# Kernel optimization log

Hardware: AMD Instinct MI355X
Metric: run time of the kernel (lower is better)

Reference implementation:

```python
import jax, jax.numpy as jnp
import numpy as np

N = 10000
E = 160000
NUM_GRAPHS = 64
HEADS = 4
HID = 256
PROJ = HEADS * HID  # 1024


def setup_inputs() -> dict:
    key = jax.random.key(0)
    ks = jax.random.split(key, 16)
    s = 0.02
    return {
        "x": jax.random.normal(ks[0], (N, 1024), jnp.float32),
        "edge_index": jax.random.randint(ks[1], (2, E), 0, N, jnp.int64) if jax.config.jax_enable_x64 else jax.random.randint(ks[1], (2, E), 0, N).astype(jnp.int32),
        "batch": jnp.sort(jax.random.randint(ks[2], (N,), 0, NUM_GRAPHS)),
        "proj_W": jax.random.normal(ks[3], (1024, PROJ), jnp.float32) * s,
        "proj_b": jnp.zeros((PROJ,), jnp.float32),
        "gat_W": jax.random.normal(ks[4], (3, PROJ, PROJ), jnp.float32) * s,
        "gat_att_src": jax.random.normal(ks[5], (3, HEADS, HID), jnp.float32) * s,
        "gat_att_dst": jax.random.normal(ks[6], (3, HEADS, HID), jnp.float32) * s,
        "gat_bias": jnp.zeros((3, PROJ), jnp.float32),
        "norm_gamma": jnp.ones((3, PROJ), jnp.float32),
        "norm_beta": jnp.zeros((3, PROJ), jnp.float32),
        "pool_W1": jax.random.normal(ks[7], (PROJ, PROJ // 2), jnp.float32) * s,
        "pool_b1": jnp.zeros((PROJ // 2,), jnp.float32),
        "pool_W2": jax.random.normal(ks[8], (PROJ // 2, 1), jnp.float32) * s,
        "pool_b2": jnp.zeros((1,), jnp.float32),
        "cls_W1": jax.random.normal(ks[9], (PROJ, PROJ // 2), jnp.float32) * s,
        "cls_b1": jnp.zeros((PROJ // 2,), jnp.float32),
        "cls_W2": jax.random.normal(ks[10], (PROJ // 2, 14), jnp.float32) * s,
        "cls_b2": jnp.zeros((14,), jnp.float32),
    }


def _segment_softmax(e, seg, num_segments):
    # numerically stable softmax over segments; e: (E, ...) scores
    m = jax.ops.segment_max(e, seg, num_segments=num_segments)
    e = jnp.exp(e - m[seg])
    s = jax.ops.segment_sum(e, seg, num_segments=num_segments)
    return e / (s[seg] + 1e-16)


def _layer_norm(x, gamma, beta):
    mu = jnp.mean(x, axis=-1, keepdims=True)
    var = jnp.var(x, axis=-1, keepdims=True)
    return (x - mu) * jax.lax.rsqrt(var + 1e-5) * gamma + beta


def _gat_conv(x, src, dst, W, a_src, a_dst, b):
    n = x.shape[0]
    h = (x @ W).reshape(n, HEADS, HID)          # (N,H,D)
    alpha_s = jnp.einsum('nhd,hd->nh', h, a_src)  # (N,H)
    alpha_d = jnp.einsum('nhd,hd->nh', h, a_dst)
    e = jax.nn.leaky_relu(alpha_s[src] + alpha_d[dst], 0.2)  # (E,H)
    alpha = _segment_softmax(e, dst, n)
    msg = h[src] * alpha[:, :, None]             # (E,H,D)
    out = jax.ops.segment_sum(msg, dst, num_segments=n)
    return out.reshape(n, PROJ) + b


def _forward(x, edge_index, batch, proj_W, proj_b, gat_W, gat_att_src, gat_att_dst,
             gat_bias, norm_gamma, norm_beta, pool_W1, pool_b1, pool_W2, pool_b2,
             cls_W1, cls_b1, cls_W2, cls_b2):
    n = x.shape[0]
    # GATConv default add_self_loops=True
    loops = jnp.arange(n, dtype=edge_index.dtype)
    src = jnp.concatenate([edge_index[0], loops])
    dst = jnp.concatenate([edge_index[1], loops])

    x = x @ proj_W + proj_b
    for i in range(3):
        h = jax.nn.elu(_gat_conv(x, src, dst, gat_W[i], gat_att_src[i], gat_att_dst[i], gat_bias[i]))
        x = _layer_norm(x + h, norm_gamma[i], norm_beta[i])  # dropout is identity in eval

    # attention pooling
    scores = (jnp.tanh(x @ pool_W1 + pool_b1) @ pool_W2 + pool_b2).squeeze(-1)  # (N,)
    w = _segment_softmax(scores, batch, NUM_GRAPHS)
    pooled = jax.ops.segment_sum(x * w[:, None], batch, num_segments=NUM_GRAPHS)  # (G,PROJ)

    hid = jax.nn.gelu(pooled @ cls_W1 + cls_b1, approximate=False)
    return hid @ cls_W2 + cls_b2  # (G,14)


def reference(x, edge_index, batch, proj_W, proj_b, gat_W, gat_att_src, gat_att_dst,
              gat_bias, norm_gamma, norm_beta, pool_W1, pool_b1, pool_W2, pool_b2,
              cls_W1, cls_b1, cls_W2, cls_b2):
    return _forward(x, edge_index, batch, proj_W, proj_b, gat_W, gat_att_src,
                    gat_att_dst, gat_bias, norm_gamma, norm_beta, pool_W1, pool_b1,
                    pool_W2, pool_b2, cls_W1, cls_b1, cls_W2, cls_b2)
```

## Files before the change

kernel.cpp:

```cpp
#include <hip/hip_runtime.h>
#include <hip/hip_bf16.h>
#include <hip/hip_fp16.h>
#include <math.h>

#define NPROJ 1024
#define NHEADS 4
#define NHID 256
#define NGRAPH 64

typedef _Float16 half8 __attribute__((ext_vector_type(8)));
typedef _Float16 half4v __attribute__((ext_vector_type(4)));
typedef float floatx4 __attribute__((ext_vector_type(4)));

#define GLD_LDS16(g, l)                                                        \
  __builtin_amdgcn_global_load_lds(                                            \
      (const __attribute__((address_space(1))) unsigned int*)(g),              \
      (__attribute__((address_space(3))) unsigned int*)(l), 16, 0, 0)

template<int ACT, int OUT>
__global__ __launch_bounds__(256, 4) void gemm_mfma(
    const _Float16* __restrict__ A, const _Float16* __restrict__ BT,
    const float* __restrict__ bias, float* __restrict__ Cf,
    _Float16* __restrict__ Ch, _Float16* __restrict__ Cl,
    int M, int Nc, int lgn, int mpad8)
{
  __shared__ __align__(16) _Float16 ldsA[128 * 64];
  __shared__ __align__(16) _Float16 ldsB[128 * 64];

  const int id  = blockIdx.x;
  const int xcd = id & 7;
  const int kk  = id >> 3;
  const int bx  = kk & ((1 << lgn) - 1);
  const int by  = xcd * mpad8 + (kk >> lgn);
  const int m0  = by * 128, n0 = bx * 128;
  if (m0 >= M) return;

  const int tid  = threadIdx.x;
  const int lane = tid & 63;
  const int wave = tid >> 6;
  const int wm = wave >> 1, wn = wave & 1;

  const int srow = tid >> 3;
  const int kc8  = (((tid & 7) ^ ((tid >> 3) & 7)) << 3);
  const int wb16 = (tid & ~63) * 16;

  floatx4 acc[4][4] = {};

  const int l15 = lane & 15;
  const int swz = (l15 & 7) << 4;
  const int kbyte0 = (lane >> 4) * 16;

  auto STAGE = [&](int t) {
    const int k0 = t << 6;
#pragma unroll
    for (int r = 0; r < 4; ++r) {
      int rowA = m0 + r * 32 + srow;
      rowA = rowA < M ? rowA : (M - 1);
      GLD_LDS16(A + (size_t)rowA * 1024 + k0 + kc8,
                (char*)ldsA + r * 4096 + wb16);
      GLD_LDS16(BT + (size_t)(n0 + r * 32 + srow) * 1024 + k0 + kc8,
                (char*)ldsB + r * 4096 + wb16);
    }
  };

  STAGE(0);
  __syncthreads();

  for (int t = 0; t < 16; ++t) {
    const int koff0 = kbyte0 ^ swz;
    half8 a0[4], b0[4];
#pragma unroll
    for (int i = 0; i < 4; ++i)
      a0[i] = *(const half8*)((const char*)ldsA +
                              (wm * 64 + i * 16 + l15) * 128 + koff0);
#pragma unroll
    for (int j = 0; j < 4; ++j)
      b0[j] = *(const half8*)((const char*)ldsB +
                              (wn * 64 + j * 16 + l15) * 128 + koff0);
#pragma unroll
    for (int i = 0; i < 4; ++i)
#pragma unroll
      for (int j = 0; j < 4; ++j)
        acc[i][j] = __builtin_amdgcn_mfma_f32_16x16x32_f16(a0[i], b0[j],
                                                           acc[i][j], 0, 0, 0);

    const int koff1 = (64 + kbyte0) ^ swz;
    half8 a1[4], b1[4];
#pragma unroll
    for (int i = 0; i < 4; ++i)
      a1[i] = *(const half8*)((const char*)ldsA +
                              (wm * 64 + i * 16 + l15) * 128 + koff1);
#pragma unroll
    for (int j = 0; j < 4; ++j)
      b1[j] = *(const half8*)((const char*)ldsB +
                              (wn * 64 + j * 16 + l15) * 128 + koff1);
    __syncthreads();
    if (t < 15) STAGE(t + 1);

#pragma unroll
    for (int i = 0; i < 4; ++i)
#pragma unroll
      for (int j = 0; j < 4; ++j)
        acc[i][j] = __builtin_amdgcn_mfma_f32_16x16x32_f16(a1[i], b1[j],
                                                           acc[i][j], 0, 0, 0);

    if (t < 15) __syncthreads();
  }

  const int rbase = (lane >> 4) * 4;
#pragma unroll
  for (int j = 0; j < 4; ++j) {
    const int col = n0 + wn * 64 + j * 16 + l15;
    const float bv = bias ? bias[col] : 0.f;
#pragma unroll
    for (int i = 0; i < 4; ++i) {
      const int gm0 = m0 + wm * 64 + i * 16 + rbase;
#pragma unroll
      for (int r = 0; r < 4; ++r) {
        const int gm = gm0 + r;
        if (gm >= M) continue;
        float v = acc[i][j][r] + bv;
        if (ACT == 1) v = tanhf(v);
        if (OUT == 1) {
          _Float16 hh = (_Float16)v;
          Ch[(size_t)gm * Nc + col] = hh;
          Cl[(size_t)gm * Nc + col] = (_Float16)(v - (float)hh);
        } else if (OUT == 2) {
          Ch[(size_t)gm * Nc + col] = (_Float16)v;
        } else {
          Cf[(size_t)gm * Nc + col] = v;
        }
      }
    }
  }
}

__global__ void k_tof16(const float* __restrict__ in, _Float16* __restrict__ h,
                        int L8) {
  int i = blockIdx.x * 256 + threadIdx.x;
  if (i >= L8) return;
  const float4* p = (const float4*)(in + (size_t)i * 8);
  float4 v0 = p[0], v1 = p[1];
  float vv[8] = {v0.x, v0.y, v0.z, v0.w, v1.x, v1.y, v1.z, v1.w};
  half8 hv;
#pragma unroll
  for (int j = 0; j < 8; ++j) hv[j] = (_Float16)vv[j];
  *(half8*)(h + (size_t)i * 8) = hv;
}

__global__ __launch_bounds__(256) void k_transT(const float* __restrict__ in,
                                                _Float16* __restrict__ hT,
                                                int K, int Nc) {
  __shared__ float t[32][33];
  const int tx = threadIdx.x & 31, ty = threadIdx.x >> 5;
  const int c0 = blockIdx.x * 32, k0 = blockIdx.y * 32;
#pragma unroll
  for (int r = 0; r < 4; ++r)
    t[ty + 8 * r][tx] = in[(size_t)(k0 + ty + 8 * r) * Nc + c0 + tx];
  __syncthreads();
#pragma unroll
  for (int r = 0; r < 4; ++r) {
    float v = t[tx][ty + 8 * r];
    int oc = c0 + ty + 8 * r;
    hT[(size_t)oc * K + k0 + tx] = (_Float16)v;
  }
}

__global__ void k_init_counts(int* cnt, int n) {
  int i = blockIdx.x * 256 + threadIdx.x;
  if (i < n) cnt[i] = 1;
}

__global__ void k_count(const int* __restrict__ dst, int* cnt, int e) {
  int i = blockIdx.x * 256 + threadIdx.x;
  if (i < e) atomicAdd(&cnt[dst[i]], 1);
}

__global__ __launch_bounds__(1024) void k_scan(const int* __restrict__ cnt,
                                               int* __restrict__ rowstart,
                                               int* __restrict__ cursor, int n) {
  __shared__ int buf[1024];
  __shared__ int carry;
  int t = threadIdx.x;
  if (t == 0) carry = 0;
  __syncthreads();
  for (int base = 0; base < n; base += 1024) {
    int x = (base + t < n) ? cnt[base + t] : 0;
    buf[t] = x;
    __syncthreads();
    for (int off = 1; off < 1024; off <<= 1) {
      int v = (t >= off) ? buf[t - off] : 0;
      __syncthreads();
      buf[t] += v;
      __syncthreads();
    }
    int c0 = carry;
    int excl = buf[t] - x + c0;
    if (base + t < n) { rowstart[base + t] = excl; cursor[base + t] = excl; }
    __syncthreads();
    if (t == 0) carry = c0 + buf[1023];
    __syncthreads();
  }
  if (t == 0) rowstart[n] = carry;
}

__global__ void k_fill(const int* __restrict__ src, const int* __restrict__ dst,
                       int* cursor, int* __restrict__ col, int e) {
  int i = blockIdx.x * 256 + threadIdx.x;
  if (i < e) {
    int p = atomicAdd(&cursor[dst[i]], 1);
    col[p] = src[i];
  }
}

__global__ void k_fill_self(int* cursor, int* __restrict__ col, int n) {
  int i = blockIdx.x * 256 + threadIdx.x;
  if (i < n) {
    int p = atomicAdd(&cursor[i], 1);
    col[p] = i;
  }
}

__global__ __launch_bounds__(256) void k_alpha(
    const _Float16* __restrict__ h, const float* __restrict__ a_src,
    const float* __restrict__ a_dst, float* __restrict__ as_out,
    float* __restrict__ ad_out) {
  int n = blockIdx.x, t = threadIdx.x;
  const int wv = t >> 6, ln = t & 63;
  const int cb = wv * 256 + 4 * ln;
  half4v v = *(const half4v*)(h + (size_t)n * NPROJ + cb);
  float4 s4 = *(const float4*)(a_src + cb);
  float4 d4 = *(const float4*)(a_dst + cb);
  float vv[4] = {(float)v[0], (float)v[1], (float)v[2], (float)v[3]};
  float ss = vv[0] * s4.x + vv[1] * s4.y + vv[2] * s4.z + vv[3] * s4.w;
  float sd = vv[0] * d4.x + vv[1] * d4.y + vv[2] * d4.z + vv[3] * d4.w;
#pragma unroll
  for (int off = 32; off > 0; off >>= 1) {
    ss += __shfl_down(ss, off);
    sd += __shfl_down(sd, off);
  }
  if (ln == 0) {
    as_out[n * 4 + wv] = ss;
    ad_out[n * 4 + wv] = sd;
  }
}

__device__ __forceinline__ float lrelu02(float x) {
  return x > 0.f ? x : 0.2f * x;
}

__global__ __launch_bounds__(256) void k_aggregate_ln(
    const _Float16* __restrict__ h, const float* __restrict__ as_,
    const float* __restrict__ ad_, const int* __restrict__ rowstart,
    const int* __restrict__ col, const float* __restrict__ bias,
    const float* __restrict__ gamma, const float* __restrict__ beta,
    _Float16* __restrict__ xh, _Float16* __restrict__ xl) {
  __shared__ float sred[8];

  const int n = blockIdx.x, t = threadIdx.x;
  const int wv = t >> 6, l = t & 63;
  const int rs = rowstart[n], re = rowstart[n + 1];
  const float adn = ad_[n * 4 + wv];

  float mx = -1e30f;
  for (int e = rs + l; e < re; e += 64)
    mx = fmaxf(mx, lrelu02(as_[(size_t)col[e] * 4 + wv] + adn));
#pragma unroll
  for (int off = 32; off > 0; off >>= 1)
    mx = fmaxf(mx, __shfl_xor(mx, off));

  float sm = 0.f;
  for (int e = rs + l; e < re; e += 64)
    sm += expf(lrelu02(as_[(size_t)col[e] * 4 + wv] + adn) - mx);
#pragma unroll
  for (int off = 32; off > 0; off >>= 1)
    sm += __shfl_xor(sm, off);
  const float Sinv = 1.f / (sm + 1e-16f);

  const int cb = wv * 256 + 4 * l;
  float acc[4] = {0.f, 0.f, 0.f, 0.f};
  for (int c0 = rs; c0 < re; c0 += 64) {
    const int idx = c0 + l;
    float w_l = 0.f;
    int s_l = 0;
    if (idx < re) {
      s_l = col[idx];
      w_l = expf(lrelu02(as_[(size_t)s_l * 4 + wv] + adn) - mx) * Sinv;
    }
    const int cnt = min(64, re - c0);
    int e = 0;
    for (; e + 3 < cnt; e += 4) {
      float w0 = __shfl(w_l, e + 0), w1 = __shfl(w_l, e + 1);
      float w2 = __shfl(w_l, e + 2), w3 = __shfl(w_l, e + 3);
      int s0 = __shfl(s_l, e + 0), s1 = __shfl(s_l, e + 1);
      int s2 = __shfl(s_l, e + 2), s3 = __shfl(s_l, e + 3);
      half4v h0 = *(const half4v*)(h + (size_t)s0 * NPROJ + cb);
      half4v h1 = *(const half4v*)(h + (size_t)s1 * NPROJ + cb);
      half4v h2 = *(const half4v*)(h + (size_t)s2 * NPROJ + cb);
      half4v h3 = *(const half4v*)(h + (size_t)s3 * NPROJ + cb);
#pragma unroll
      for (int j = 0; j < 4; ++j) {
        acc[j] = fmaf(w0, (float)h0[j], acc[j]);
        acc[j] = fmaf(w1, (float)h1[j], acc[j]);
        acc[j] = fmaf(w2, (float)h2[j], acc[j]);
        acc[j] = fmaf(w3, (float)h3[j], acc[j]);
      }
    }
    for (; e < cnt; ++e) {
      const float w = __shfl(w_l, e);
      const int s = __shfl(s_l, e);
      half4v hv = *(const half4v*)(h + (size_t)s * NPROJ + cb);
      acc[0] = fmaf(w, (float)hv[0], acc[0]);
      acc[1] = fmaf(w, (float)hv[1], acc[1]);
      acc[2] = fmaf(w, (float)hv[2], acc[2]);
      acc[3] = fmaf(w, (float)hv[3], acc[3]);
    }
  }

  const size_t base = (size_t)n * NPROJ + cb;
  float4 b4 = *(const float4*)(bias + cb);
  float bb[4] = {b4.x, b4.y, b4.z, b4.w};
  half4v xhv = *(const half4v*)(xh + base);
  half4v xlv = *(const half4v*)(xl + base);
  float v[4];
  float sum = 0.f, sumsq = 0.f;
#pragma unroll
  for (int j = 0; j < 4; ++j) {
    float u = acc[j] + bb[j];
    u = u > 0.f ? u : expm1f(u);
    u += (float)xhv[j] + (float)xlv[j];
    v[j] = u;
    sum += u;
    sumsq += u * u;
  }
#pragma unroll
  for (int off = 32; off > 0; off >>= 1) {
    sum += __shfl_xor(sum, off);
    sumsq += __shfl_xor(sumsq, off);
  }
  if (l == 0) {
    sred[wv] = sum;
    sred[4 + wv] = sumsq;
  }
  __syncthreads();
  const float tsum = sred[0] + sred[1] + sred[2] + sred[3];
  const float tssq = sred[4] + sred[5] + sred[6] + sred[7];
  const float mu = tsum * (1.f / 1024.f);
  const float var = tssq * (1.f / 1024.f) - mu * mu;
  const float rstd = rsqrtf(var + 1e-5f);

  float4 g4 = *(const float4*)(gamma + cb);
  float4 e4 = *(const float4*)(beta + cb);
  float gg[4] = {g4.x, g4.y, g4.z, g4.w};
  float ee[4] = {e4.x, e4.y, e4.z, e4.w};
  half4v oh, ol;
#pragma unroll
  for (int j = 0; j < 4; ++j) {
    float y = (v[j] - mu) * rstd * gg[j] + ee[j];
    _Float16 hh = (_Float16)y;
    oh[j] = hh;
    ol[j] = (_Float16)(y - (float)hh);
  }
  *(half4v*)(xh + base) = oh;
  *(half4v*)(xl + base) = ol;
}

__global__ void k_scores(const float* __restrict__ tb,
                         const float* __restrict__ W2,
                         const float* __restrict__ b2,
                         float* __restrict__ scores, int N) {
  int n = blockIdx.x, lane = threadIdx.x;
  float s = 0.f;
  for (int k = lane; k < 512; k += 64) s = fmaf(tb[(size_t)n * 512 + k], W2[k], s);
  for (int off = 32; off > 0; off >>= 1) s += __shfl_down(s, off);
  if (lane == 0) scores[n] = s + b2[0];
}

__global__ void k_grange_init(int* gstart, int* gend, int N) {
  int g = threadIdx.x;
  if (g < NGRAPH) { gstart[g] = N; gend[g] = 0; }
}

__global__ void k_grange_mark(const int* __restrict__ batch, int* gstart,
                              int* gend, int N) {
  int n = blockIdx.x * 256 + threadIdx.x;
  if (n >= N) return;
  int b = batch[n];
  if (n == 0 || batch[n - 1] != b) gstart[b] = n;
  if (n == N - 1 || batch[n + 1] != b) gend[b] = n + 1;
}

__global__ __launch_bounds__(256) void k_pool(
    const float* __restrict__ scores, const _Float16* __restrict__ xh,
    const _Float16* __restrict__ xl, const int* __restrict__ gstart,
    const int* __restrict__ gend, float* __restrict__ pooled) {
  __shared__ float red[256];
  __shared__ float wt[256];
  __shared__ float m_s, s_s;
  int g = blockIdx.x, t = threadIdx.x;
  int rs = gstart[g], re = gend[g];

  float mx = -1e30f;
  for (int i = rs + t; i < re; i += 256) mx = fmaxf(mx, scores[i]);
  red[t] = mx;
  __syncthreads();
  for (int s = 128; s > 0; s >>= 1) {
    if (t < s) red[t] = fmaxf(red[t], red[t + s]);
    __syncthreads();
  }
  if (t == 0) m_s = red[0];
  __syncthreads();
  float m = m_s;

  float sm = 0.f;
  for (int i = rs + t; i < re; i += 256) sm += expf(scores[i] - m);
  red[t] = sm;
  __syncthreads();
  for (int s = 128; s > 0; s >>= 1) {
    if (t < s) red[t] += red[t + s];
    __syncthreads();
  }
  if (t == 0) s_s = red[0] + 1e-16f;
  __syncthreads();
  float sden = s_s;

  float acc[4] = {0.f, 0.f, 0.f, 0.f};
  for (int c0 = rs; c0 < re; c0 += 256) {
    int cnt = min(256, re - c0);
    if (t < cnt) wt[t] = expf(scores[c0 + t] - m) / sden;
    __syncthreads();
    for (int e = 0; e < cnt; ++e) {
      float w = wt[e];
      size_t base = (size_t)(c0 + e) * NPROJ + 4 * t;
      half4v hv = *(const half4v*)(xh + base);
      half4v lv = *(const half4v*)(xl + base);
#pragma unroll
      for (int j = 0; j < 4; ++j)
        acc[j] = fmaf(w, (float)hv[j] + (float)lv[j], acc[j]);
    }
    __syncthreads();
  }
#pragma unroll
  for (int j = 0; j < 4; ++j) pooled[(size_t)g * NPROJ + 4 * t + j] = acc[j];
}

__global__ __launch_bounds__(256) void k_cls1(const float* __restrict__ pooled,
                                              const float* __restrict__ W1,
                                              const float* __restrict__ b1,
                                              float* __restrict__ hid) {
  __shared__ float p[1024];
  int g = blockIdx.y;
  int colc = blockIdx.x * 256 + threadIdx.x;
  for (int k = threadIdx.x; k < 1024; k += 256) p[k] = pooled[(size_t)g * 1024 + k];
  __syncthreads();
  float s = 0.f;
  for (int k = 0; k < 1024; ++k) s = fmaf(p[k], W1[(size_t)k * 512 + colc], s);
  s += b1[colc];
  s = 0.5f * s * (1.f + erff(s * 0.70710678118654752f));
  hid[(size_t)g * 512 + colc] = s;
}

__global__ void k_cls2(const float* __restrict__ hid,
                       const float* __restrict__ W2,
                       const float* __restrict__ b2, float* __restrict__ out) {
  int o = blockIdx.x, g = blockIdx.y, lane = threadIdx.x;
  float s = 0.f;
  for (int k = lane; k < 512; k += 64) s = fmaf(hid[(size_t)g * 512 + k], W2[k * 14 + o], s);
  for (int off = 32; off > 0; off >>= 1) s += __shfl_down(s, off);
  if (lane == 0) out[g * 14 + o] = s + b2[o];
}

extern "C" void kernel_launch(void* const* d_in, const int* in_sizes, int n_in,
                              void* d_out, int out_size, void* d_ws, size_t ws_size,
                              hipStream_t stream) {
  const float* x_in   = (const float*)d_in[0];
  const int*   eidx   = (const int*)d_in[1];
  const int*   batch  = (const int*)d_in[2];
  const float* proj_W = (const float*)d_in[3];
  const float* proj_b = (const float*)d_in[4];
  const float* gat_W  = (const float*)d_in[5];
  const float* a_src  = (const float*)d_in[6];
  const float* a_dst  = (const float*)d_in[7];
  const float* gat_b  = (const float*)d_in[8];
  const float* gamma  = (const float*)d_in[9];
  const float* beta   = (const float*)d_in[10];
  const float* pW1    = (const float*)d_in[11];
  const float* pb1    = (const float*)d_in[12];
  const float* pW2    = (const float*)d_in[13];
  const float* pb2    = (const float*)d_in[14];
  const float* cW1    = (const float*)d_in[15];
  const float* cb1    = (const float*)d_in[16];
  const float* cW2    = (const float*)d_in[17];
  const float* cb2    = (const float*)d_in[18];
  float* out = (float*)d_out;

  const int N = in_sizes[0] / NPROJ;
  const int E = in_sizes[1] / 2;
  const int Etot = E + N;

  char* ws = (char*)d_ws;
  size_t off = 0;
  auto alloc = [&](size_t bytes) -> void* {
    void* p = ws + off;
    off = (off + bytes + 255) & ~(size_t)255;
    return p;
  };
  _Float16* xh   = (_Float16*)alloc((size_t)N * NPROJ * 2);
  _Float16* xl   = (_Float16*)alloc((size_t)N * NPROJ * 2);
  _Float16* hf   = (_Float16*)alloc((size_t)N * NPROJ * 2);
  float*    hb   = (float*)alloc((size_t)N * NPROJ * 4);
  _Float16* pjh  = (_Float16*)alloc((size_t)NPROJ * NPROJ * 2);
  _Float16* gwh  = (_Float16*)alloc((size_t)3 * NPROJ * NPROJ * 2);
  _Float16* pwh  = (_Float16*)alloc((size_t)512 * NPROJ * 2);
  float* asb     = (float*)alloc((size_t)N * 4 * 4);
  float* adb     = (float*)alloc((size_t)N * 4 * 4);
  int*   cnt     = (int*)alloc((size_t)N * 4);
  int*   rowst   = (int*)alloc((size_t)(N + 1) * 4);
  int*   cursor  = (int*)alloc((size_t)N * 4);
  int*   ccol    = (int*)alloc((size_t)Etot * 4);
  float* scores  = (float*)alloc((size_t)N * 4);
  int*   gstart  = (int*)alloc(NGRAPH * 4);
  int*   gend    = (int*)alloc(NGRAPH * 4);
  float* pooled  = (float*)alloc((size_t)NGRAPH * NPROJ * 4);
  float* hid     = (float*)alloc((size_t)NGRAPH * 512 * 4);

  const int* esrc = eidx;
  const int* edst = eidx + E;

  k_init_counts<<<(N + 255) / 256, 256, 0, stream>>>(cnt, N);
  k_count<<<(E + 255) / 256, 256, 0, stream>>>(edst, cnt, E);
  k_scan<<<1, 1024, 0, stream>>>(cnt, rowst, cursor, N);
  k_fill<<<(E + 255) / 256, 256, 0, stream>>>(esrc, edst, cursor, ccol, E);
  k_fill_self<<<(N + 255) / 256, 256, 0, stream>>>(cursor, ccol, N);

  k_transT<<<dim3(32, 32), 256, 0, stream>>>(proj_W, pjh, NPROJ, NPROJ);
  for (int i = 0; i < 3; ++i)
    k_transT<<<dim3(32, 32), 256, 0, stream>>>(gat_W + (size_t)i * NPROJ * NPROJ,
                                               gwh + (size_t)i * NPROJ * NPROJ,
                                               NPROJ, NPROJ);
  k_transT<<<dim3(16, 32), 256, 0, stream>>>(pW1, pwh, NPROJ, 512);

  _Float16* inh = (_Float16*)hb;
  k_tof16<<<((N * NPROJ / 8) + 255) / 256, 256, 0, stream>>>(x_in, inh,
                                                             N * NPROJ / 8);
  const int MB = (N + 127) / 128;
  const int mpad8 = (MB + 7) / 8;
  const dim3 grid8(8 * mpad8 * 8);
  const dim3 grid4(4 * mpad8 * 8);
  gemm_mfma<0, 1><<<grid8, 256, 0, stream>>>(
      inh, pjh, proj_b, nullptr, xh, xl, N, NPROJ, 3, mpad8);

  for (int i = 0; i < 3; ++i) {
    gemm_mfma<0, 2><<<grid8, 256, 0, stream>>>(
        xh, gwh + (size_t)i * NPROJ * NPROJ,
        nullptr, nullptr, hf, nullptr, N, NPROJ, 3, mpad8);
    k_alpha<<<N, 256, 0, stream>>>(hf, a_src + i * NPROJ, a_dst + i * NPROJ, asb, adb);
    k_aggregate_ln<<<N, 256, 0, stream>>>(hf, asb, adb, rowst, ccol,
                                          gat_b + i * NPROJ, gamma + i * NPROJ,
                                          beta + i * NPROJ, xh, xl);
  }

  float* tb = hb;
  gemm_mfma<1, 0><<<grid4, 256, 0, stream>>>(
      xh, pwh, pb1, tb, nullptr, nullptr, N, 512, 2, mpad8);
  k_scores<<<N, 64, 0, stream>>>(tb, pW2, pb2, scores, N);
  k_grange_init<<<1, 64, 0, stream>>>(gstart, gend, N);
  k_grange_mark<<<(N + 255) / 256, 256, 0, stream>>>(batch, gstart, gend, N);
  k_pool<<<NGRAPH, 256, 0, stream>>>(scores, xh, xl, gstart, gend, pooled);

  k_cls1<<<dim3(2, NGRAPH), 256, 0, stream>>>(pooled, cW1, cb1, hid);
  k_cls2<<<dim3(14, NGRAPH), 64, 0, stream>>>(hid, cW2, cb2, out);
}
```

Measured before the change: 505.5 us.

## Parallelize CSR scan, pack two nodes per alpha block, unroll aggregation by six

```diff
diff --git a/kernel.cpp b/kernel.cpp
--- a/kernel.cpp
+++ b/kernel.cpp
@@ -176,32 +176,49 @@
   if (i < e) atomicAdd(&cnt[dst[i]], 1);
 }
 
-__global__ __launch_bounds__(1024) void k_scan(const int* __restrict__ cnt,
-                                               int* __restrict__ rowstart,
-                                               int* __restrict__ cursor, int n) {
-  __shared__ int buf[1024];
-  __shared__ int carry;
-  int t = threadIdx.x;
-  if (t == 0) carry = 0;
-  __syncthreads();
-  for (int base = 0; base < n; base += 1024) {
-    int x = (base + t < n) ? cnt[base + t] : 0;
-    buf[t] = x;
-    __syncthreads();
-    for (int off = 1; off < 1024; off <<= 1) {
-      int v = (t >= off) ? buf[t - off] : 0;
-      __syncthreads();
-      buf[t] += v;
-      __syncthreads();
-    }
-    int c0 = carry;
-    int excl = buf[t] - x + c0;
-    if (base + t < n) { rowstart[base + t] = excl; cursor[base + t] = excl; }
-    __syncthreads();
-    if (t == 0) carry = c0 + buf[1023];
-    __syncthreads();
-  }
-  if (t == 0) rowstart[n] = carry;
+__global__ __launch_bounds__(256) void k_scan1(int* __restrict__ cnt,
+                                               int* __restrict__ bsum, int n) {
+  __shared__ int wsum[4];
+  const int b = blockIdx.x, t = threadIdx.x, i = b * 256 + t;
+  const int x = (i < n) ? cnt[i] : 0;
+  int v = x;
+#pragma unroll
+  for (int off = 1; off < 64; off <<= 1) {
+    int u = __shfl_up(v, off);
+    if ((t & 63) >= off) v += u;
+  }
+  if ((t & 63) == 63) wsum[t >> 6] = v;
+  __syncthreads();
+  int wo = 0;
+#pragma unroll
+  for (int w = 0; w < 4; ++w) wo += (w < (t >> 6)) ? wsum[w] : 0;
+  const int incl = v + wo;
+  if (i < n) cnt[i] = incl - x;
+  if (t == 255) bsum[b] = incl;
+}
+
+__global__ void k_scan2(int* __restrict__ bsum, int nb) {
+  const int t = threadIdx.x;
+  const int x = (t < nb) ? bsum[t] : 0;
+  int v = x;
+#pragma unroll
+  for (int off = 1; off < 64; off <<= 1) {
+    int u = __shfl_up(v, off);
+    if (t >= off) v += u;
+  }
+  if (t < nb) bsum[t] = v - x;
+}
+
+__global__ void k_scan3(const int* __restrict__ cnt, const int* __restrict__ bsum,
+                        int* __restrict__ rowstart, int* __restrict__ cursor,
+                        int n, int etot) {
+  const int i = blockIdx.x * 256 + threadIdx.x;
+  if (i < n) {
+    const int v = cnt[i] + bsum[i >> 8];
+    rowstart[i] = v;
+    cursor[i] = v;
+  }
+  if (i == 0) rowstart[n] = etot;
 }
 
 __global__ void k_fill(const int* __restrict__ src, const int* __restrict__ dst,
@@ -224,24 +241,35 @@
 __global__ __launch_bounds__(256) void k_alpha(
     const _Float16* __restrict__ h, const float* __restrict__ a_src,
     const float* __restrict__ a_dst, float* __restrict__ as_out,
-    float* __restrict__ ad_out) {
-  int n = blockIdx.x, t = threadIdx.x;
-  const int wv = t >> 6, ln = t & 63;
-  const int cb = wv * 256 + 4 * ln;
-  half4v v = *(const half4v*)(h + (size_t)n * NPROJ + cb);
-  float4 s4 = *(const float4*)(a_src + cb);
-  float4 d4 = *(const float4*)(a_dst + cb);
-  float vv[4] = {(float)v[0], (float)v[1], (float)v[2], (float)v[3]};
-  float ss = vv[0] * s4.x + vv[1] * s4.y + vv[2] * s4.z + vv[3] * s4.w;
-  float sd = vv[0] * d4.x + vv[1] * d4.y + vv[2] * d4.z + vv[3] * d4.w;
-#pragma unroll
-  for (int off = 32; off > 0; off >>= 1) {
-    ss += __shfl_down(ss, off);
-    sd += __shfl_down(sd, off);
-  }
-  if (ln == 0) {
-    as_out[n * 4 + wv] = ss;
-    ad_out[n * 4 + wv] = sd;
+    float* __restrict__ ad_out, int N) {
+  const int t = threadIdx.x;
+  const int w = t >> 6, l = t & 63;
+  const int node = blockIdx.x * 2 + (w >> 1);
+  if (node >= N) return;
+  const int head = (w & 1) * 2 + (l >> 5);
+  const int cb = head * 256 + (l & 31) * 8;
+  half8 v = *(const half8*)(h + (size_t)node * NPROJ + cb);
+  float4 s0 = *(const float4*)(a_src + cb);
+  float4 s1 = *(const float4*)(a_src + cb + 4);
+  float4 d0 = *(const float4*)(a_dst + cb);
+  float4 d1 = *(const float4*)(a_dst + cb + 4);
+  float sv[8] = {s0.x, s0.y, s0.z, s0.w, s1.x, s1.y, s1.z, s1.w};
+  float dv[8] = {d0.x, d0.y, d0.z, d0.w, d1.x, d1.y, d1.z, d1.w};
+  float ss = 0.f, sd = 0.f;
+#pragma unroll
+  for (int j = 0; j < 8; ++j) {
+    float f = (float)v[j];
+    ss = fmaf(f, sv[j], ss);
+    sd = fmaf(f, dv[j], sd);
+  }
+#pragma unroll
+  for (int off = 1; off <= 16; off <<= 1) {
+    ss += __shfl_xor(ss, off);
+    sd += __shfl_xor(sd, off);
+  }
+  if ((l & 31) == 0) {
+    as_out[node * 4 + head] = ss;
+    ad_out[node * 4 + head] = sd;
   }
 }
 
@@ -289,21 +317,27 @@
     }
     const int cnt = min(64, re - c0);
     int e = 0;
-    for (; e + 3 < cnt; e += 4) {
+    for (; e + 5 < cnt; e += 6) {
       float w0 = __shfl(w_l, e + 0), w1 = __shfl(w_l, e + 1);
       float w2 = __shfl(w_l, e + 2), w3 = __shfl(w_l, e + 3);
+      float w4 = __shfl(w_l, e + 4), w5 = __shfl(w_l, e + 5);
       int s0 = __shfl(s_l, e + 0), s1 = __shfl(s_l, e + 1);
       int s2 = __shfl(s_l, e + 2), s3 = __shfl(s_l, e + 3);
+      int s4 = __shfl(s_l, e + 4), s5 = __shfl(s_l, e + 5);
       half4v h0 = *(const half4v*)(h + (size_t)s0 * NPROJ + cb);
       half4v h1 = *(const half4v*)(h + (size_t)s1 * NPROJ + cb);
       half4v h2 = *(const half4v*)(h + (size_t)s2 * NPROJ + cb);
       half4v h3 = *(const half4v*)(h + (size_t)s3 * NPROJ + cb);
+      half4v h4 = *(const half4v*)(h + (size_t)s4 * NPROJ + cb);
+      half4v h5 = *(const half4v*)(h + (size_t)s5 * NPROJ + cb);
 #pragma unroll
       for (int j = 0; j < 4; ++j) {
         acc[j] = fmaf(w0, (float)h0[j], acc[j]);
         acc[j] = fmaf(w1, (float)h1[j], acc[j]);
         acc[j] = fmaf(w2, (float)h2[j], acc[j]);
         acc[j] = fmaf(w3, (float)h3[j], acc[j]);
+        acc[j] = fmaf(w4, (float)h4[j], acc[j]);
+        acc[j] = fmaf(w5, (float)h5[j], acc[j]);
       }
     }
     for (; e < cnt; ++e) {
@@ -497,6 +531,7 @@
   const int N = in_sizes[0] / NPROJ;
   const int E = in_sizes[1] / 2;
   const int Etot = E + N;
+  const int NB = (N + 255) / 256;
 
   char* ws = (char*)d_ws;
   size_t off = 0;
@@ -515,6 +550,7 @@
   float* asb     = (float*)alloc((size_t)N * 4 * 4);
   float* adb     = (float*)alloc((size_t)N * 4 * 4);
   int*   cnt     = (int*)alloc((size_t)N * 4);
+  int*   bsum    = (int*)alloc(64 * 4);
   int*   rowst   = (int*)alloc((size_t)(N + 1) * 4);
   int*   cursor  = (int*)alloc((size_t)N * 4);
   int*   ccol    = (int*)alloc((size_t)Etot * 4);
@@ -527,11 +563,13 @@
   const int* esrc = eidx;
   const int* edst = eidx + E;
 
-  k_init_counts<<<(N + 255) / 256, 256, 0, stream>>>(cnt, N);
+  k_init_counts<<<NB, 256, 0, stream>>>(cnt, N);
   k_count<<<(E + 255) / 256, 256, 0, stream>>>(edst, cnt, E);
-  k_scan<<<1, 1024, 0, stream>>>(cnt, rowst, cursor, N);
+  k_scan1<<<NB, 256, 0, stream>>>(cnt, bsum, N);
+  k_scan2<<<1, 64, 0, stream>>>(bsum, NB);
+  k_scan3<<<NB, 256, 0, stream>>>(cnt, bsum, rowst, cursor, N, Etot);
   k_fill<<<(E + 255) / 256, 256, 0, stream>>>(esrc, edst, cursor, ccol, E);
-  k_fill_self<<<(N + 255) / 256, 256, 0, stream>>>(cursor, ccol, N);
+  k_fill_self<<<NB, 256, 0, stream>>>(cursor, ccol, N);
 
   k_transT<<<dim3(32, 32), 256, 0, stream>>>(proj_W, pjh, NPROJ, NPROJ);
   for (int i = 0; i < 3; ++i)
@@ -554,7 +592,8 @@
     gemm_mfma<0, 2><<<grid8, 256, 0, stream>>>(
         xh, gwh + (size_t)i * NPROJ * NPROJ,
         nullptr, nullptr, hf, nullptr, N, NPROJ, 3, mpad8);
-    k_alpha<<<N, 256, 0, stream>>>(hf, a_src + i * NPROJ, a_dst + i * NPROJ, asb, adb);
+    k_alpha<<<(N + 1) / 2, 256, 0, stream>>>(hf, a_src + i * NPROJ,
+                                             a_dst + i * NPROJ, asb, adb, N);
     k_aggregate_ln<<<N, 256, 0, stream>>>(hf, asb, adb, rowst, ccol,
                                           gat_b + i * NPROJ, gamma + i * NPROJ,
                                           beta + i * NPROJ, xh, xl);
@@ -565,7 +604,7 @@
       xh, pwh, pb1, tb, nullptr, nullptr, N, 512, 2, mpad8);
   k_scores<<<N, 64, 0, stream>>>(tb, pW2, pb2, scores, N);
   k_grange_init<<<1, 64, 0, stream>>>(gstart, gend, N);
-  k_grange_mark<<<(N + 255) / 256, 256, 0, stream>>>(batch, gstart, gend, N);
+  k_grange_mark<<<NB, 256, 0, stream>>>(batch, gstart, gend, N);
   k_pool<<<NGRAPH, 256, 0, stream>>>(scores, xh, xl, gstart, gend, pooled);
 
   k_cls1<<<dim3(2, NGRAPH), 256, 0, stream>>>(pooled, cW1, cb1, hid);
```

Result: faster. 484.0 us (-4.3%).
